# Kernel tuning notes

Measured on AMD Instinct MI355X. Metric: run time of the kernel, lower is better.

Reference implementation:

```python
import jax, jax.numpy as jnp
import numpy as np

N, E, D, ED, H, G, OUT = 50000, 800000, 128, 50, 128, 256, 1
NEG_SLOPE = 0.2  # PyG GATConv default LeakyReLU slope


def setup_inputs() -> dict:
    key = jax.random.key(0)
    ks = jax.random.split(key, 20)
    p = lambda k, shape: jax.random.normal(k, shape, jnp.float32) * 0.05
    inp = {
        "x": jax.random.normal(ks[0], (N, D), jnp.float32),
        "edge_index": jax.random.randint(ks[1], (2, E), 0, N, dtype=jnp.int32),
        "edge_attr": jax.random.uniform(ks[2], (E, ED), jnp.float32),
        "batch": jnp.sort(jax.random.randint(ks[3], (N,), 0, G, dtype=jnp.int32)),
        # conv1 (GATConv, heads=1): node lin, att_src/att_dst, edge lin, att_edge, bias
        "W1": p(ks[4], (D, H)), "as1": p(ks[5], (H,)), "ad1": p(ks[6], (H,)),
        "We1": p(ks[7], (ED, H)), "ae1": p(ks[8], (H,)), "b1": jnp.zeros((H,), jnp.float32),
        # conv2
        "W2": p(ks[9], (H, H)), "as2": p(ks[10], (H,)), "ad2": p(ks[11], (H,)),
        "We2": p(ks[12], (ED, H)), "ae2": p(ks[13], (H,)), "b2": jnp.zeros((H,), jnp.float32),
        # final Linear
        "Wfc": p(ks[14], (H, OUT)), "bfc": jnp.zeros((OUT,), jnp.float32),
    }
    return inp


def _gat(x, edge_index, edge_attr, W, a_src, a_dst, We, a_edge, b):
    """PyG GATConv, heads=1, concat=True, add_self_loops=True (fill_value='mean')."""
    n = x.shape[0]
    loop = jnp.arange(n, dtype=edge_index.dtype)
    src = jnp.concatenate([edge_index[0], loop])          # [E+N]
    dst = jnp.concatenate([edge_index[1], loop])          # [E+N]
    ea = jnp.concatenate(
        [edge_attr, jnp.broadcast_to(edge_attr.mean(axis=0), (n, edge_attr.shape[1]))], axis=0)
    h = x @ W                                              # [N, H]
    al_s = h @ a_src                                       # [N]
    al_d = h @ a_dst                                       # [N]
    al_e = (ea @ We) @ a_edge                              # [E+N]
    alpha = jax.nn.leaky_relu(al_s[src] + al_d[dst] + al_e, NEG_SLOPE)
    # segment softmax over incoming edges of each dst node
    amax = jax.ops.segment_max(alpha, dst, num_segments=n)
    amax = jnp.where(jnp.isfinite(amax), amax, 0.0)
    ex = jnp.exp(alpha - amax[dst])
    denom = jax.ops.segment_sum(ex, dst, num_segments=n)
    coef = ex / denom[dst]                                 # self-loops guarantee denom > 0
    out = jax.ops.segment_sum(h[src] * coef[:, None], dst, num_segments=n)
    return out + b


def reference(x, edge_index, edge_attr, batch,
              W1, as1, ad1, We1, ae1, b1,
              W2, as2, ad2, We2, ae2, b2,
              Wfc, bfc):
    h = jax.nn.relu(_gat(x, edge_index, edge_attr, W1, as1, ad1, We1, ae1, b1))
    h = jax.nn.relu(_gat(h, edge_index, edge_attr, W2, as2, ad2, We2, ae2, b2))
    # global_mean_pool over batch ids
    sums = jax.ops.segment_sum(h, batch, num_segments=G)
    cnt = jax.ops.segment_sum(jnp.ones((h.shape[0],), h.dtype), batch, num_segments=G)
    pooled = sums / jnp.maximum(cnt, 1.0)[:, None]
    return pooled @ Wfc + bfc
```

## Files before the change

### kernel.cpp

```cpp
#include <hip/hip_runtime.h>
#include <hip/hip_bf16.h>
#include <cstdint>
#include <cstddef>

#define NEG_SLOPE 0.2f
#define HD 128
#define ED 50

static inline int ceil_div(int a, int b){ return (a + b - 1) / b; }

__global__ void k_init(int* __restrict__ counts, float* __restrict__ pool_sum,
                       float* __restrict__ pool_cnt, float* __restrict__ al_e_sum,
                       int n, int g)
{
  int i = blockIdx.x * blockDim.x + threadIdx.x;
  int stride = gridDim.x * blockDim.x;
  for (int idx = i; idx < n; idx += stride) counts[idx] = 0;
  if (i < g) { pool_sum[i] = 0.f; pool_cnt[i] = 0.f; }
  if (i < 2) al_e_sum[i] = 0.f;
}

__global__ void k_wevec(const float* __restrict__ We1, const float* __restrict__ ae1,
                        const float* __restrict__ We2, const float* __restrict__ ae2,
                        float* __restrict__ we_vec )
{
  int l = blockIdx.x, d = threadIdx.x;
  const float* We = l ? We2 : We1;
  const float* ae = l ? ae2 : ae1;
  if (d < ED) {
    float s = 0.f;
    for (int k = 0; k < HD; ++k) s += We[d * HD + k] * ae[k];
    we_vec[l * 64 + d] = s;
  }
}

__global__ __launch_bounds__(256) void k_edge_ale(
    const float* __restrict__ ea, const float* __restrict__ we_vec,
    float* __restrict__ al_e1, float* __restrict__ al_e2,
    float* __restrict__ al_e_sum, int E)
{
  __shared__ float sh[256 * 51];
  __shared__ float wv1[ED], wv2[ED];
  __shared__ float ws1[4], ws2[4];
  int tid = threadIdx.x;
  if (tid < ED) { wv1[tid] = we_vec[tid]; wv2[tid] = we_vec[64 + tid]; }

  int e0 = blockIdx.x * 256;
  int cnt = min(256, E - e0);
  int elems = (cnt > 0) ? cnt * ED : 0;
  const float* base = ea + (size_t)e0 * ED;
  const float4* base4 = (const float4*)base;
  int n4 = elems >> 2;
  for (int i = tid; i < n4; i += 256) {
    float4 v = base4[i];
    int f = i << 2;
    int le = f / ED; int d = f - le * ED; sh[le * 51 + d] = v.x;
    f++; le = f / ED; d = f - le * ED;    sh[le * 51 + d] = v.y;
    f++; le = f / ED; d = f - le * ED;    sh[le * 51 + d] = v.z;
    f++; le = f / ED; d = f - le * ED;    sh[le * 51 + d] = v.w;
  }
  for (int i = (n4 << 2) + tid; i < elems; i += 256) {
    int le = i / ED, d = i - le * ED;
    sh[le * 51 + d] = base[i];
  }
  __syncthreads();

  float a1 = 0.f, a2 = 0.f;
  if (tid < cnt) {
    const float* row = &sh[tid * 51];
#pragma unroll
    for (int d = 0; d < ED; ++d) {
      float v = row[d];
      a1 = fmaf(v, wv1[d], a1);
      a2 = fmaf(v, wv2[d], a2);
    }
    al_e1[e0 + tid] = a1;
    al_e2[e0 + tid] = a2;
  }
  float s1 = a1, s2 = a2;
#pragma unroll
  for (int o = 32; o; o >>= 1) { s1 += __shfl_xor(s1, o); s2 += __shfl_xor(s2, o); }
  int lane = tid & 63, wave = tid >> 6;
  if (lane == 0) { ws1[wave] = s1; ws2[wave] = s2; }
  __syncthreads();
  if (tid == 0) {
    atomicAdd(&al_e_sum[0], ws1[0] + ws1[1] + ws1[2] + ws1[3]);
    atomicAdd(&al_e_sum[1], ws2[0] + ws2[1] + ws2[2] + ws2[3]);
  }
}

__global__ void k_loop_e(const float* __restrict__ al_e_sum, float* __restrict__ loop_e, float invE)
{
  int t = threadIdx.x;
  if (t < 2) loop_e[t] = al_e_sum[t] * invE;
}

__global__ void k_count(const int* __restrict__ dst, int* __restrict__ counts, int E)
{
  int i = blockIdx.x * blockDim.x + threadIdx.x;
  int stride = gridDim.x * blockDim.x;
  for (; i < E; i += stride) atomicAdd(&counts[dst[i]], 1);
}

__global__ __launch_bounds__(1024) void k_scanA(const int* __restrict__ counts, int* __restrict__ tmp,
                                                int* __restrict__ chunk_sums, int n)
{
  __shared__ int sd[1024];
  int tid = threadIdx.x;
  int i = blockIdx.x * 1024 + tid;
  int v = (i < n) ? counts[i] : 0;
  sd[tid] = v;
  __syncthreads();
  for (int off = 1; off < 1024; off <<= 1) {
    int t = (tid >= off) ? sd[tid - off] : 0;
    __syncthreads();
    sd[tid] += t;
    __syncthreads();
  }
  if (i < n) tmp[i] = sd[tid] - v;
  if (tid == 1023) chunk_sums[blockIdx.x] = sd[1023];
}

__global__ void k_scanB(const int* __restrict__ chunk_sums, int* __restrict__ chunk_off,
                        int nchunks, int* __restrict__ row_off_end)
{
  if (threadIdx.x == 0) {
    int run = 0;
    for (int c = 0; c < nchunks; ++c) { chunk_off[c] = run; run += chunk_sums[c]; }
    *row_off_end = run;
  }
}

__global__ __launch_bounds__(1024) void k_scanC(const int* __restrict__ tmp, const int* __restrict__ chunk_off,
                                                int* __restrict__ row_off, int* __restrict__ cursor, int n)
{
  int i = blockIdx.x * 1024 + threadIdx.x;
  if (i < n) {
    int v = tmp[i] + chunk_off[blockIdx.x];
    row_off[i] = v;
    cursor[i] = v;
  }
}

__global__ void k_fill(const int* __restrict__ dst, int* __restrict__ cursor,
                       int* __restrict__ csr, int E)
{
  int i = blockIdx.x * blockDim.x + threadIdx.x;
  int stride = gridDim.x * blockDim.x;
  for (; i < E; i += stride) {
    int d = dst[i];
    int pos = atomicAdd(&cursor[d], 1);
    csr[pos] = i;
  }
}

__global__ __launch_bounds__(256) void k_gemm128(const float* __restrict__ A,
                                                 const float* __restrict__ W,
                                                 float* __restrict__ C, int M)
{
  __shared__ float Wl[HD * HD];
  int tid = threadIdx.x;
  {
    const float4* W4 = (const float4*)W;
    float4* Wl4 = (float4*)Wl;
#pragma unroll
    for (int i = 0; i < 16; ++i) Wl4[tid + i * 256] = W4[tid + i * 256];
  }
  __syncthreads();

  int q = tid & 31;
  int rg = tid >> 5;
  int row0 = blockIdx.x * 32 + rg * 4;

  const float* xr0 = A + (size_t)(row0 + 0 < M ? row0 + 0 : M - 1) * HD;
  const float* xr1 = A + (size_t)(row0 + 1 < M ? row0 + 1 : M - 1) * HD;
  const float* xr2 = A + (size_t)(row0 + 2 < M ? row0 + 2 : M - 1) * HD;
  const float* xr3 = A + (size_t)(row0 + 3 < M ? row0 + 3 : M - 1) * HD;

  float4 acc0 = {0.f,0.f,0.f,0.f}, acc1 = acc0, acc2 = acc0, acc3 = acc0;

  for (int k = 0; k < HD; k += 4) {
    const float* wk = &Wl[k * HD + 4 * q];
    float4 w0 = *(const float4*)(wk);
    float4 w1 = *(const float4*)(wk + HD);
    float4 w2 = *(const float4*)(wk + 2 * HD);
    float4 w3 = *(const float4*)(wk + 3 * HD);
    float4 xa = *(const float4*)(xr0 + k);
    float4 xb = *(const float4*)(xr1 + k);
    float4 xc = *(const float4*)(xr2 + k);
    float4 xd = *(const float4*)(xr3 + k);
#define ROWFMA(ACC, XV)                                                   \
    ACC.x = fmaf(XV.x, w0.x, ACC.x); ACC.x = fmaf(XV.y, w1.x, ACC.x);     \
    ACC.x = fmaf(XV.z, w2.x, ACC.x); ACC.x = fmaf(XV.w, w3.x, ACC.x);     \
    ACC.y = fmaf(XV.x, w0.y, ACC.y); ACC.y = fmaf(XV.y, w1.y, ACC.y);     \
    ACC.y = fmaf(XV.z, w2.y, ACC.y); ACC.y = fmaf(XV.w, w3.y, ACC.y);     \
    ACC.z = fmaf(XV.x, w0.z, ACC.z); ACC.z = fmaf(XV.y, w1.z, ACC.z);     \
    ACC.z = fmaf(XV.z, w2.z, ACC.z); ACC.z = fmaf(XV.w, w3.z, ACC.z);     \
    ACC.w = fmaf(XV.x, w0.w, ACC.w); ACC.w = fmaf(XV.y, w1.w, ACC.w);     \
    ACC.w = fmaf(XV.z, w2.w, ACC.w); ACC.w = fmaf(XV.w, w3.w, ACC.w);
    ROWFMA(acc0, xa)
    ROWFMA(acc1, xb)
    ROWFMA(acc2, xc)
    ROWFMA(acc3, xd)
#undef ROWFMA
  }

  if (row0 + 0 < M) *(float4*)&C[(size_t)(row0 + 0) * HD + 4 * q] = acc0;
  if (row0 + 1 < M) *(float4*)&C[(size_t)(row0 + 1) * HD + 4 * q] = acc1;
  if (row0 + 2 < M) *(float4*)&C[(size_t)(row0 + 2) * HD + 4 * q] = acc2;
  if (row0 + 3 < M) *(float4*)&C[(size_t)(row0 + 3) * HD + 4 * q] = acc3;
}

__global__ void k_node_dots(const float* __restrict__ h, const float* __restrict__ a_s,
                            const float* __restrict__ a_d, float* __restrict__ al_s,
                            float* __restrict__ al_d, int n)
{
  int wave = threadIdx.x >> 6, lane = threadIdx.x & 63;
  int node = blockIdx.x * 4 + wave;
  if (node >= n) return;
  const float* hr = h + (size_t)node * HD;
  float v1 = hr[lane], v2 = hr[lane + 64];
  float ss = v1 * a_s[lane] + v2 * a_s[lane + 64];
  float dd = v1 * a_d[lane] + v2 * a_d[lane + 64];
#pragma unroll
  for (int o = 32; o; o >>= 1) { ss += __shfl_xor(ss, o); dd += __shfl_xor(dd, o); }
  if (lane == 0) { al_s[node] = ss; al_d[node] = dd; }
}

template <bool FUSE>
__global__ __launch_bounds__(256) void k_agg(
    const int* __restrict__ row_off, const int* __restrict__ csr,
    const int* __restrict__ src,
    const float* __restrict__ al_s, const float* __restrict__ al_d,
    const float* __restrict__ al_e, const float* __restrict__ loop_e, int le_idx,
    const float* __restrict__ h, const float* __restrict__ bias,
    float* __restrict__ o,
    const float* __restrict__ Wfc, const int* __restrict__ batchv,
    float* __restrict__ pool_sum, float* __restrict__ pool_cnt,
    int n_nodes)
{
  int wave = threadIdx.x >> 6, lane = threadIdx.x & 63;
  int n = blockIdx.x * 4 + wave;
  if (n >= n_nodes) return;

  float led  = loop_e[le_idx];
  float ad_n = al_d[n];

  float a0 = al_s[n] + ad_n + led;
  a0 = a0 > 0.f ? a0 : NEG_SLOPE * a0;
  float w = __expf(a0);
  const float* hn = h + (size_t)n * HD;
  float acc1 = w * hn[lane];
  float acc2 = w * hn[lane + 64];
  float s = w;

  int k0 = row_off[n], k1 = row_off[n + 1];
  for (int k = k0; k < k1; ++k) {
    int e  = csr[k];
    int sn = src[e];
    float a = al_s[sn] + ad_n + al_e[e];
    a = a > 0.f ? a : NEG_SLOPE * a;
    float we = __expf(a);
    s += we;
    const float* hs = h + (size_t)sn * HD;
    acc1 += we * hs[lane];
    acc2 += we * hs[lane + 64];
  }

  float inv = 1.0f / s;
  float o1v = fmaxf(acc1 * inv + bias[lane], 0.f);
  float o2v = fmaxf(acc2 * inv + bias[lane + 64], 0.f);

  if (FUSE) {
    float t = o1v * Wfc[lane] + o2v * Wfc[lane + 64];
#pragma unroll
    for (int ofs = 32; ofs; ofs >>= 1) t += __shfl_xor(t, ofs);
    if (lane == 0) {
      int g = batchv[n];
      atomicAdd(&pool_sum[g], t);
      atomicAdd(&pool_cnt[g], 1.0f);
    }
  } else {
    float* orow = o + (size_t)n * HD;
    orow[lane] = o1v;
    orow[lane + 64] = o2v;
  }
}

__global__ void k_final(const float* __restrict__ pool_sum, const float* __restrict__ pool_cnt,
                        const float* __restrict__ bfc, float* __restrict__ out, int g)
{
  int i = blockIdx.x * blockDim.x + threadIdx.x;
  if (i < g) out[i] = pool_sum[i] / fmaxf(pool_cnt[i], 1.f) + bfc[0];
}

extern "C" void kernel_launch(void* const* d_in, const int* in_sizes, int n_in,
                              void* d_out, int out_size, void* d_ws, size_t ws_size,
                              hipStream_t stream)
{
  const float* x       = (const float*)d_in[0];
  const int*   ei      = (const int*)d_in[1];
  const float* ea      = (const float*)d_in[2];
  const int*   batchv  = (const int*)d_in[3];
  const float* W1  = (const float*)d_in[4];
  const float* as1 = (const float*)d_in[5];
  const float* ad1 = (const float*)d_in[6];
  const float* We1 = (const float*)d_in[7];
  const float* ae1 = (const float*)d_in[8];
  const float* b1  = (const float*)d_in[9];
  const float* W2  = (const float*)d_in[10];
  const float* as2 = (const float*)d_in[11];
  const float* ad2 = (const float*)d_in[12];
  const float* We2 = (const float*)d_in[13];
  const float* ae2 = (const float*)d_in[14];
  const float* b2  = (const float*)d_in[15];
  const float* Wfc = (const float*)d_in[16];
  const float* bfc = (const float*)d_in[17];
  float* out = (float*)d_out;

  const int N = in_sizes[0] / HD;
  const int E = in_sizes[1] / 2;
  const int G = out_size;
  const int* src = ei;
  const int* dst = ei + E;

  char* p = (char*)d_ws;
  auto alloc = [&](size_t bytes) -> void* {
    void* r = (void*)p;
    p += (bytes + 255) & ~(size_t)255;
    return r;
  };
  float* hA       = (float*)alloc((size_t)N * HD * 4);
  float* oB       = (float*)alloc((size_t)N * HD * 4);
  float* al_e1    = (float*)alloc((size_t)E * 4);
  float* al_e2    = (float*)alloc((size_t)E * 4);
  float* al_s     = (float*)alloc((size_t)N * 4);
  float* al_d     = (float*)alloc((size_t)N * 4);
  int*   counts   = (int*)alloc((size_t)N * 4);
  int*   row_off  = (int*)alloc((size_t)(N + 1) * 4);
  int*   tmp_scan = (int*)alloc((size_t)N * 4);
  int*   chunk_sums = (int*)alloc(64 * 4);
  int*   chunk_off  = (int*)alloc(64 * 4);
  int*   csr      = (int*)alloc((size_t)E * 4);
  float* we_vec   = (float*)alloc(2 * 64 * 4);
  float* al_e_sum = (float*)alloc(2 * 4);
  float* loop_e   = (float*)alloc(2 * 4);
  float* pool_sum = (float*)alloc((size_t)G * 4);
  float* pool_cnt = (float*)alloc((size_t)G * 4);
  (void)ws_size; (void)n_in;

  const int nchunks = ceil_div(N, 1024);

  k_init<<<ceil_div(N, 256), 256, 0, stream>>>(counts, pool_sum, pool_cnt, al_e_sum, N, G);
  k_wevec<<<2, 64, 0, stream>>>(We1, ae1, We2, ae2, we_vec);
  k_edge_ale<<<ceil_div(E, 256), 256, 0, stream>>>(ea, we_vec, al_e1, al_e2, al_e_sum, E);
  k_loop_e<<<1, 64, 0, stream>>>(al_e_sum, loop_e, 1.0f / (float)E);
  k_count<<<2048, 256, 0, stream>>>(dst, counts, E);
  k_scanA<<<nchunks, 1024, 0, stream>>>(counts, tmp_scan, chunk_sums, N);
  k_scanB<<<1, 64, 0, stream>>>(chunk_sums, chunk_off, nchunks, &row_off[N]);
  k_scanC<<<nchunks, 1024, 0, stream>>>(tmp_scan, chunk_off, row_off, counts, N);
  k_fill<<<2048, 256, 0, stream>>>(dst, counts, csr, E);

  k_gemm128<<<ceil_div(N, 32), 256, 0, stream>>>(x, W1, hA, N);
  k_node_dots<<<ceil_div(N, 4), 256, 0, stream>>>(hA, as1, ad1, al_s, al_d, N);
  k_agg<false><<<ceil_div(N, 4), 256, 0, stream>>>(row_off, csr, src, al_s, al_d,
      al_e1, loop_e, 0, hA, b1, oB, nullptr, nullptr, nullptr, nullptr, N);

  k_gemm128<<<ceil_div(N, 32), 256, 0, stream>>>(oB, W2, hA, N);
  k_node_dots<<<ceil_div(N, 4), 256, 0, stream>>>(hA, as2, ad2, al_s, al_d, N);
  k_agg<true><<<ceil_div(N, 4), 256, 0, stream>>>(row_off, csr, src, al_s, al_d,
      al_e2, loop_e, 1, hA, b2, nullptr, Wfc, batchv, pool_sum, pool_cnt, N);

  k_final<<<1, 256, 0, stream>>>(pool_sum, pool_cnt, bfc, out, G);
}
```

Before: 906.7 us.

## Precompute per-edge attention weights in CSR order and fuse node dots into GEMM

The CSR fill now writes a packed per-edge record (src, dst, both layers' edge logits) in dst-sorted order. A new per-layer edge kernel computes exp(leakyrelu) weights into a compact (src, weight) array, so the aggregation no longer chases csr->src->al_e indirections or evaluates exp inside the serial per-node loop. The aggregation loop is unrolled by four to keep more gathers in flight, and the node attention dot products move into the GEMM epilogue, removing a separate kernel and a reread of h. In exchange it adds an extra E-sized pass per layer and larger scratch buffers.

Result: faster. 872.8 us (-3.7%).

```diff
diff --git a/kernel.cpp b/kernel.cpp
--- a/kernel.cpp
+++ b/kernel.cpp
@@ -142,21 +142,32 @@
   }
 }
 
-__global__ void k_fill(const int* __restrict__ dst, int* __restrict__ cursor,
-                       int* __restrict__ csr, int E)
+__global__ void k_fill(const int* __restrict__ src, const int* __restrict__ dst,
+                       const float* __restrict__ al_e1, const float* __restrict__ al_e2,
+                       int* __restrict__ cursor, float4* __restrict__ edata, int E)
 {
   int i = blockIdx.x * blockDim.x + threadIdx.x;
   int stride = gridDim.x * blockDim.x;
   for (; i < E; i += stride) {
     int d = dst[i];
     int pos = atomicAdd(&cursor[d], 1);
-    csr[pos] = i;
+    float4 v;
+    v.x = __int_as_float(src[i]);
+    v.y = __int_as_float(d);
+    v.z = al_e1[i];
+    v.w = al_e2[i];
+    edata[pos] = v;
   }
 }
 
 __global__ __launch_bounds__(256) void k_gemm128(const float* __restrict__ A,
                                                  const float* __restrict__ W,
-                                                 float* __restrict__ C, int M)
+                                                 float* __restrict__ C,
+                                                 const float* __restrict__ a_s,
+                                                 const float* __restrict__ a_d,
+                                                 float* __restrict__ al_s,
+                                                 float* __restrict__ al_d,
+                                                 int M)
 {
   __shared__ float Wl[HD * HD];
   int tid = threadIdx.x;
@@ -209,30 +220,52 @@
   if (row0 + 1 < M) *(float4*)&C[(size_t)(row0 + 1) * HD + 4 * q] = acc1;
   if (row0 + 2 < M) *(float4*)&C[(size_t)(row0 + 2) * HD + 4 * q] = acc2;
   if (row0 + 3 < M) *(float4*)&C[(size_t)(row0 + 3) * HD + 4 * q] = acc3;
-}
-
-__global__ void k_node_dots(const float* __restrict__ h, const float* __restrict__ a_s,
-                            const float* __restrict__ a_d, float* __restrict__ al_s,
-                            float* __restrict__ al_d, int n)
-{
-  int wave = threadIdx.x >> 6, lane = threadIdx.x & 63;
-  int node = blockIdx.x * 4 + wave;
-  if (node >= n) return;
-  const float* hr = h + (size_t)node * HD;
-  float v1 = hr[lane], v2 = hr[lane + 64];
-  float ss = v1 * a_s[lane] + v2 * a_s[lane + 64];
-  float dd = v1 * a_d[lane] + v2 * a_d[lane + 64];
+
+  float4 asv = *(const float4*)&a_s[4 * q];
+  float4 adv = *(const float4*)&a_d[4 * q];
+  float ps0 = acc0.x*asv.x + acc0.y*asv.y + acc0.z*asv.z + acc0.w*asv.w;
+  float ps1 = acc1.x*asv.x + acc1.y*asv.y + acc1.z*asv.z + acc1.w*asv.w;
+  float ps2 = acc2.x*asv.x + acc2.y*asv.y + acc2.z*asv.z + acc2.w*asv.w;
+  float ps3 = acc3.x*asv.x + acc3.y*asv.y + acc3.z*asv.z + acc3.w*asv.w;
+  float pd0 = acc0.x*adv.x + acc0.y*adv.y + acc0.z*adv.z + acc0.w*adv.w;
+  float pd1 = acc1.x*adv.x + acc1.y*adv.y + acc1.z*adv.z + acc1.w*adv.w;
+  float pd2 = acc2.x*adv.x + acc2.y*adv.y + acc2.z*adv.z + acc2.w*adv.w;
+  float pd3 = acc3.x*adv.x + acc3.y*adv.y + acc3.z*adv.z + acc3.w*adv.w;
 #pragma unroll
-  for (int o = 32; o; o >>= 1) { ss += __shfl_xor(ss, o); dd += __shfl_xor(dd, o); }
-  if (lane == 0) { al_s[node] = ss; al_d[node] = dd; }
+  for (int o = 16; o; o >>= 1) {
+    ps0 += __shfl_xor(ps0, o); ps1 += __shfl_xor(ps1, o);
+    ps2 += __shfl_xor(ps2, o); ps3 += __shfl_xor(ps3, o);
+    pd0 += __shfl_xor(pd0, o); pd1 += __shfl_xor(pd1, o);
+    pd2 += __shfl_xor(pd2, o); pd3 += __shfl_xor(pd3, o);
+  }
+  if (q == 0) {
+    if (row0 + 0 < M) { al_s[row0 + 0] = ps0; al_d[row0 + 0] = pd0; }
+    if (row0 + 1 < M) { al_s[row0 + 1] = ps1; al_d[row0 + 1] = pd1; }
+    if (row0 + 2 < M) { al_s[row0 + 2] = ps2; al_d[row0 + 2] = pd2; }
+    if (row0 + 3 < M) { al_s[row0 + 3] = ps3; al_d[row0 + 3] = pd3; }
+  }
+}
+
+__global__ __launch_bounds__(256) void k_edge_w(
+    const float4* __restrict__ edata, const float* __restrict__ al_s,
+    const float* __restrict__ al_d, float2* __restrict__ pack, int E, int layer)
+{
+  int k = blockIdx.x * 256 + threadIdx.x;
+  if (k >= E) return;
+  float4 v = edata[k];
+  int sn = __float_as_int(v.x);
+  int dn = __float_as_int(v.y);
+  float ale = layer ? v.w : v.z;
+  float a = al_s[sn] + al_d[dn] + ale;
+  a = a > 0.f ? a : NEG_SLOPE * a;
+  pack[k] = make_float2(v.x, __expf(a));
 }
 
 template <bool FUSE>
 __global__ __launch_bounds__(256) void k_agg(
-    const int* __restrict__ row_off, const int* __restrict__ csr,
-    const int* __restrict__ src,
+    const int* __restrict__ row_off, const float2* __restrict__ pack,
     const float* __restrict__ al_s, const float* __restrict__ al_d,
-    const float* __restrict__ al_e, const float* __restrict__ loop_e, int le_idx,
+    const float* __restrict__ loop_e, int le_idx,
     const float* __restrict__ h, const float* __restrict__ bias,
     float* __restrict__ o,
     const float* __restrict__ Wfc, const int* __restrict__ batchv,
@@ -243,10 +276,7 @@
   int n = blockIdx.x * 4 + wave;
   if (n >= n_nodes) return;
 
-  float led  = loop_e[le_idx];
-  float ad_n = al_d[n];
-
-  float a0 = al_s[n] + ad_n + led;
+  float a0 = al_s[n] + al_d[n] + loop_e[le_idx];
   a0 = a0 > 0.f ? a0 : NEG_SLOPE * a0;
   float w = __expf(a0);
   const float* hn = h + (size_t)n * HD;
@@ -254,17 +284,32 @@
   float acc2 = w * hn[lane + 64];
   float s = w;
 
-  int k0 = row_off[n], k1 = row_off[n + 1];
-  for (int k = k0; k < k1; ++k) {
-    int e  = csr[k];
-    int sn = src[e];
-    float a = al_s[sn] + ad_n + al_e[e];
-    a = a > 0.f ? a : NEG_SLOPE * a;
-    float we = __expf(a);
-    s += we;
-    const float* hs = h + (size_t)sn * HD;
-    acc1 += we * hs[lane];
-    acc2 += we * hs[lane + 64];
+  int k0 = row_off[n];
+  int cnt = row_off[n + 1] - k0;
+  const float2* pk = pack + k0;
+  int k = 0;
+  for (; k + 4 <= cnt; k += 4) {
+    float2 p0 = pk[k], p1 = pk[k + 1], p2 = pk[k + 2], p3 = pk[k + 3];
+    const float* h0 = h + (size_t)__float_as_int(p0.x) * HD;
+    const float* h1 = h + (size_t)__float_as_int(p1.x) * HD;
+    const float* h2 = h + (size_t)__float_as_int(p2.x) * HD;
+    const float* h3 = h + (size_t)__float_as_int(p3.x) * HD;
+    float v0a = h0[lane], v0b = h0[lane + 64];
+    float v1a = h1[lane], v1b = h1[lane + 64];
+    float v2a = h2[lane], v2b = h2[lane + 64];
+    float v3a = h3[lane], v3b = h3[lane + 64];
+    s += p0.y + p1.y + p2.y + p3.y;
+    acc1 = fmaf(p0.y, v0a, acc1); acc2 = fmaf(p0.y, v0b, acc2);
+    acc1 = fmaf(p1.y, v1a, acc1); acc2 = fmaf(p1.y, v1b, acc2);
+    acc1 = fmaf(p2.y, v2a, acc1); acc2 = fmaf(p2.y, v2b, acc2);
+    acc1 = fmaf(p3.y, v3a, acc1); acc2 = fmaf(p3.y, v3b, acc2);
+  }
+  for (; k < cnt; ++k) {
+    float2 p = pk[k];
+    const float* hs = h + (size_t)__float_as_int(p.x) * HD;
+    s += p.y;
+    acc1 = fmaf(p.y, hs[lane], acc1);
+    acc2 = fmaf(p.y, hs[lane + 64], acc2);
   }
 
   float inv = 1.0f / s;
@@ -330,23 +375,24 @@
     p += (bytes + 255) & ~(size_t)255;
     return r;
   };
-  float* hA       = (float*)alloc((size_t)N * HD * 4);
-  float* oB       = (float*)alloc((size_t)N * HD * 4);
-  float* al_e1    = (float*)alloc((size_t)E * 4);
-  float* al_e2    = (float*)alloc((size_t)E * 4);
-  float* al_s     = (float*)alloc((size_t)N * 4);
-  float* al_d     = (float*)alloc((size_t)N * 4);
-  int*   counts   = (int*)alloc((size_t)N * 4);
-  int*   row_off  = (int*)alloc((size_t)(N + 1) * 4);
-  int*   tmp_scan = (int*)alloc((size_t)N * 4);
-  int*   chunk_sums = (int*)alloc(64 * 4);
-  int*   chunk_off  = (int*)alloc(64 * 4);
-  int*   csr      = (int*)alloc((size_t)E * 4);
-  float* we_vec   = (float*)alloc(2 * 64 * 4);
-  float* al_e_sum = (float*)alloc(2 * 4);
-  float* loop_e   = (float*)alloc(2 * 4);
-  float* pool_sum = (float*)alloc((size_t)G * 4);
-  float* pool_cnt = (float*)alloc((size_t)G * 4);
+  float*  hA       = (float*)alloc((size_t)N * HD * 4);
+  float*  oB       = (float*)alloc((size_t)N * HD * 4);
+  float*  al_e1    = (float*)alloc((size_t)E * 4);
+  float*  al_e2    = (float*)alloc((size_t)E * 4);
+  float*  al_s     = (float*)alloc((size_t)N * 4);
+  float*  al_d     = (float*)alloc((size_t)N * 4);
+  int*    counts   = (int*)alloc((size_t)N * 4);
+  int*    row_off  = (int*)alloc((size_t)(N + 1) * 4);
+  int*    tmp_scan = (int*)alloc((size_t)N * 4);
+  int*    chunk_sums = (int*)alloc(64 * 4);
+  int*    chunk_off  = (int*)alloc(64 * 4);
+  float4* edata    = (float4*)alloc((size_t)E * 16);
+  float2* pack     = (float2*)alloc((size_t)E * 8);
+  float*  we_vec   = (float*)alloc(2 * 64 * 4);
+  float*  al_e_sum = (float*)alloc(2 * 4);
+  float*  loop_e   = (float*)alloc(2 * 4);
+  float*  pool_sum = (float*)alloc((size_t)G * 4);
+  float*  pool_cnt = (float*)alloc((size_t)G * 4);
   (void)ws_size; (void)n_in;
 
   const int nchunks = ceil_div(N, 1024);
@@ -359,17 +405,17 @@
   k_scanA<<<nchunks, 1024, 0, stream>>>(counts, tmp_scan, chunk_sums, N);
   k_scanB<<<1, 64, 0, stream>>>(chunk_sums, chunk_off, nchunks, &row_off[N]);
   k_scanC<<<nchunks, 1024, 0, stream>>>(tmp_scan, chunk_off, row_off, counts, N);
-  k_fill<<<2048, 256, 0, stream>>>(dst, counts, csr, E);
-
-  k_gemm128<<<ceil_div(N, 32), 256, 0, stream>>>(x, W1, hA, N);
-  k_node_dots<<<ceil_div(N, 4), 256, 0, stream>>>(hA, as1, ad1, al_s, al_d, N);
-  k_agg<false><<<ceil_div(N, 4), 256, 0, stream>>>(row_off, csr, src, al_s, al_d,
-      al_e1, loop_e, 0, hA, b1, oB, nullptr, nullptr, nullptr, nullptr, N);
-
-  k_gemm128<<<ceil_div(N, 32), 256, 0, stream>>>(oB, W2, hA, N);
-  k_node_dots<<<ceil_div(N, 4), 256, 0, stream>>>(hA, as2, ad2, al_s, al_d, N);
-  k_agg<true><<<ceil_div(N, 4), 256, 0, stream>>>(row_off, csr, src, al_s, al_d,
-      al_e2, loop_e, 1, hA, b2, nullptr, Wfc, batchv, pool_sum, pool_cnt, N);
+  k_fill<<<2048, 256, 0, stream>>>(src, dst, al_e1, al_e2, counts, edata, E);
+
+  k_gemm128<<<ceil_div(N, 32), 256, 0, stream>>>(x, W1, hA, as1, ad1, al_s, al_d, N);
+  k_edge_w<<<ceil_div(E, 256), 256, 0, stream>>>(edata, al_s, al_d, pack, E, 0);
+  k_agg<false><<<ceil_div(N, 4), 256, 0, stream>>>(row_off, pack, al_s, al_d,
+      loop_e, 0, hA, b1, oB, nullptr, nullptr, nullptr, nullptr, N);
+
+  k_gemm128<<<ceil_div(N, 32), 256, 0, stream>>>(oB, W2, hA, as2, ad2, al_s, al_d, N);
+  k_edge_w<<<ceil_div(E, 256), 256, 0, stream>>>(edata, al_s, al_d, pack, E, 1);
+  k_agg<true><<<ceil_div(N, 4), 256, 0, stream>>>(row_off, pack, al_s, al_d,
+      loop_e, 1, hA, b2, nullptr, Wfc, batchv, pool_sum, pool_cnt, N);
 
   k_final<<<1, 256, 0, stream>>>(pool_sum, pool_cnt, bfc, out, G);
 }
```
